# Kernel tuning notes

Measured on AMD Instinct MI355X. Metric: run time of the kernel, lower is better.

Reference implementation:

```python
import jax, jax.numpy as jnp
import numpy as np

N = 50000
E = 800000
DIN = 64
DOUT = 64
H = 4
C = DOUT // H
EPS = 1e-5


def setup_inputs() -> dict:
    key = jax.random.key(0)
    ks = jax.random.split(key, 40)
    inp = {}
    inp["x"] = jax.random.normal(ks[0], (N, DIN), jnp.float32)
    inp["edge_index"] = jax.random.randint(ks[1], (2, E), 0, N, dtype=jnp.int32)
    inp["edge_weight"] = jax.random.uniform(ks[2], (E,), jnp.float32)
    inp["edge_attr"] = jax.random.normal(ks[3], (E, 1), jnp.float32)
    k = 4
    for i in range(2):
        din = DIN if i == 0 else DOUT
        s = din ** -0.5
        inp[f"gcn_w{i}"] = jax.random.normal(ks[k], (din, DOUT), jnp.float32) * s; k += 1
        inp[f"gcn_b{i}"] = jnp.zeros((DOUT,), jnp.float32)
        inp[f"res_w{i}"] = jax.random.normal(ks[k], (din, DOUT), jnp.float32) * s; k += 1
        inp[f"res_b{i}"] = jnp.zeros((DOUT,), jnp.float32)
        inp[f"ln_g{i}"] = jnp.ones((DOUT,), jnp.float32)
        inp[f"ln_b{i}"] = jnp.zeros((DOUT,), jnp.float32)
        sg = DOUT ** -0.5
        inp[f"gat_w{i}"] = jax.random.normal(ks[k], (DOUT, H * C), jnp.float32) * sg; k += 1
        inp[f"gat_b{i}"] = jnp.zeros((H * C,), jnp.float32)
        inp[f"att_src{i}"] = jax.random.normal(ks[k], (H, C), jnp.float32) * (C ** -0.5); k += 1
        inp[f"att_dst{i}"] = jax.random.normal(ks[k], (H, C), jnp.float32) * (C ** -0.5); k += 1
        inp[f"att_e{i}"] = jax.random.normal(ks[k], (H, C), jnp.float32) * (C ** -0.5); k += 1
        inp[f"ew_w{i}"] = jax.random.normal(ks[k], (1, H * C), jnp.float32); k += 1
    return inp


def _gcn(x, src0, dst0, ew, W, b):
    n = x.shape[0]
    sl = jnp.arange(n, dtype=src0.dtype)
    src = jnp.concatenate([src0, sl])
    dst = jnp.concatenate([dst0, sl])
    w = jnp.concatenate([ew, jnp.ones((n,), ew.dtype)])  # self-loop weight 1
    deg = jax.ops.segment_sum(w, dst, num_segments=n)
    dinv = jnp.where(deg > 0, jax.lax.rsqrt(deg), 0.0)
    norm = dinv[src] * w * dinv[dst]
    h = x @ W  # [n, DOUT]
    out = jax.ops.segment_sum(h[src] * norm[:, None], dst, num_segments=n)
    return out + b


def _gat(x, src0, dst0, ea, W, b, a_src, a_dst, a_e, We):
    n = x.shape[0]
    sl = jnp.arange(n, dtype=src0.dtype)
    src = jnp.concatenate([src0, sl])
    dst = jnp.concatenate([dst0, sl])
    loop_attr = jnp.broadcast_to(ea.mean(axis=0, keepdims=True), (n, ea.shape[1]))
    ea2 = jnp.concatenate([ea, loop_attr], axis=0)  # fill_value='mean'
    xl = (x @ W).reshape(n, H, C)
    a_s = (xl * a_src).sum(-1)  # [n,H]
    a_d = (xl * a_dst).sum(-1)
    a_ee = ((ea2 @ We).reshape(-1, H, C) * a_e).sum(-1)  # [E2,H]
    alpha = jax.nn.leaky_relu(a_s[src] + a_d[dst] + a_ee, 0.2)
    m = jax.ops.segment_max(alpha, dst, num_segments=n)
    e = jnp.exp(alpha - m[dst])
    s = jax.ops.segment_sum(e, dst, num_segments=n)
    alpha = e / (s[dst] + 1e-16)
    out = jax.ops.segment_sum(xl[src] * alpha[:, :, None], dst, num_segments=n)
    return out.reshape(n, H * C) + b


def _ln(x, g, b):
    mu = x.mean(-1, keepdims=True)
    v = ((x - mu) ** 2).mean(-1, keepdims=True)
    return (x - mu) * jax.lax.rsqrt(v + EPS) * g + b


def reference(x, edge_index, edge_weight, edge_attr,
              gcn_w0, gcn_b0, res_w0, res_b0, ln_g0, ln_b0,
              gat_w0, gat_b0, att_src0, att_dst0, att_e0, ew_w0,
              gcn_w1, gcn_b1, res_w1, res_b1, ln_g1, ln_b1,
              gat_w1, gat_b1, att_src1, att_dst1, att_e1, ew_w1):
    src0, dst0 = edge_index[0], edge_index[1]
    layers = [
        (gcn_w0, gcn_b0, res_w0, res_b0, ln_g0, ln_b0, gat_w0, gat_b0, att_src0, att_dst0, att_e0, ew_w0),
        (gcn_w1, gcn_b1, res_w1, res_b1, ln_g1, ln_b1, gat_w1, gat_b1, att_src1, att_dst1, att_e1, ew_w1),
    ]
    for (gw, gb, rw, rb, lg, lb, Wg, bg, a_s, a_d, a_e, We) in layers:
        residual = x @ rw + rb
        x = jax.nn.silu(_gcn(x, src0, dst0, edge_weight, gw, gb)) + residual
        x = _ln(x, lg, lb)
        x = jax.nn.silu(_gat(x, src0, dst0, edge_attr, Wg, bg, a_s, a_d, a_e, We)) + x
    return x  # down_sample=False -> Identity
```

## Files before the change

kernel.cpp:

```cpp
#include <hip/hip_runtime.h>
#include <hip/hip_fp16.h>

#define NN 50000
#define NE 800000
#define D 64
#define EPS 1e-5f
#define NT 3125
#define NB1 250
#define EPB 3200
#define NBIN 196
#define STOT 49152
#define SBLK 192

typedef unsigned short ushort_t;
typedef unsigned int uint_t;
typedef __attribute__((ext_vector_type(8))) short bf16x8;
typedef __attribute__((ext_vector_type(4))) float f32x4;

__device__ __forceinline__ float wave_sum64(float v) {
#pragma unroll
  for (int m = 1; m <= 32; m <<= 1) v += __shfl_xor(v, m, 64);
  return v;
}
__device__ __forceinline__ float group_sum16(float v) {
#pragma unroll
  for (int m = 1; m <= 8; m <<= 1) v += __shfl_xor(v, m, 64);
  return v;
}
__device__ __forceinline__ float silu_f(float v) { return v / (1.f + __expf(-v)); }
__device__ __forceinline__ float lrelu_f(float v) { return v >= 0.f ? v : 0.2f * v; }
__device__ __forceinline__ ushort_t f2b(float x) {
  unsigned u = __float_as_uint(x);
  return (ushort_t)((u + 0x7FFFu + ((u >> 16) & 1u)) >> 16);
}
__device__ __forceinline__ float b2f(ushort_t u) {
  return __uint_as_float(((unsigned)u) << 16);
}
__device__ __forceinline__ ushort_t f2h(float x) {
  return __half_as_ushort(__float2half_rn(x));
}
__device__ __forceinline__ float h2f(unsigned u) {
  return __half2float(__ushort_as_half((ushort_t)(u & 0xFFFFu)));
}
__device__ __forceinline__ float sel4(float a, float b, float c, float d, int h) {
  float ab = (h & 1) ? b : a;
  float cd = (h & 1) ? d : c;
  return (h & 2) ? cd : ab;
}
__device__ __forceinline__ bf16x8 pack8(float4 a, float4 b) {
  bf16x8 r;
  r[0] = (short)f2b(a.x); r[1] = (short)f2b(a.y);
  r[2] = (short)f2b(a.z); r[3] = (short)f2b(a.w);
  r[4] = (short)f2b(b.x); r[5] = (short)f2b(b.y);
  r[6] = (short)f2b(b.z); r[7] = (short)f2b(b.w);
  return r;
}


__global__ void __launch_bounds__(256) k_hist196(const int* __restrict__ ei,
                                                 int* __restrict__ histG) {
  __shared__ int h[NBIN];
  int blk = blockIdx.x;
  for (int j = threadIdx.x; j < NBIN; j += 256) h[j] = 0;
  __syncthreads();
  int e0 = blk * EPB;
  for (int e = e0 + threadIdx.x; e < e0 + EPB; e += 256)
    atomicAdd(&h[ei[NE + e] >> 8], 1);
  __syncthreads();
  for (int j = threadIdx.x; j < NBIN; j += 256) histG[j * NB1 + blk] = h[j];
}

__global__ void __launch_bounds__(256) k_scanMA(int* __restrict__ histG,
                                                int* __restrict__ bsum) {
  __shared__ int sm[256];
  int j = threadIdx.x;
  int i = blockIdx.x * 256 + j;
  const int TOT = NBIN * NB1;
  int v = (i < TOT) ? histG[i] : 0;
  sm[j] = v;
  __syncthreads();
  for (int off = 1; off < 256; off <<= 1) {
    int t = (j >= off) ? sm[j - off] : 0;
    __syncthreads();
    sm[j] += t;
    __syncthreads();
  }
  if (i < TOT) histG[i] = sm[j] - v;
  if (j == 255) bsum[blockIdx.x] = sm[255];
}

__global__ void __launch_bounds__(256) k_scanMB(int* __restrict__ bsum,
                                                float* __restrict__ scal) {
  __shared__ int sm[256];
  int j = threadIdx.x;
  for (int t = j; t < 1024; t += 256) scal[t] = 0.f;
  int v = (j < SBLK) ? bsum[j] : 0;
  sm[j] = v;
  __syncthreads();
  for (int off = 1; off < 256; off <<= 1) {
    int t = (j >= off) ? sm[j - off] : 0;
    __syncthreads();
    sm[j] += t;
    __syncthreads();
  }
  if (j < SBLK) bsum[j] = sm[j] - v;
}

__global__ void __launch_bounds__(256) k_scanMC(int* __restrict__ histG,
                                                const int* __restrict__ bsum) {
  int i = blockIdx.x * 256 + threadIdx.x;
  const int TOT = NBIN * NB1;
  if (i < TOT) histG[i] += bsum[i >> 8];
}

__global__ void __launch_bounds__(256) k_part(
    const int* __restrict__ ei, const float* __restrict__ ew,
    const float* __restrict__ ea, const int* __restrict__ histG,
    uint2* __restrict__ rectmp, float* __restrict__ scal) {
  __shared__ int cur[NBIN];
  int blk = blockIdx.x;
  for (int j = threadIdx.x; j < NBIN; j += 256) cur[j] = histG[j * NB1 + blk];
  __syncthreads();
  int e0 = blk * EPB;
  float asum = 0.f;
  for (int e = e0 + threadIdx.x; e < e0 + EPB; e += 256) {
    int src = ei[e];
    int dst = ei[NE + e];
    float w = ew[e];
    float a = ea[e];
    asum += a;
    int slot = atomicAdd(&cur[dst >> 8], 1);
    uint2 r;
    r.x = (uint_t)(src & 0xFFFF) | ((uint_t)f2h(w) << 16);
    r.y = (uint_t)(dst & 0xFF) | ((uint_t)f2h(a) << 16);
    rectmp[slot] = r;
  }
  float s = wave_sum64(asum);
  if ((threadIdx.x & 63) == 0) {
    int slot = (blk * 4 + (threadIdx.x >> 6)) & 63;
    atomicAdd(&scal[(size_t)slot * 16], s);
  }
}

__global__ void __launch_bounds__(256) k_sortfin(
    const uint2* __restrict__ rectmp, const int* __restrict__ histG,
    uint2* __restrict__ rec, int* __restrict__ rs) {
  __shared__ int cnt[256], sc[256], cur[256];
  int b = blockIdx.x;
  int t = threadIdx.x;
  int lo = histG[b * NB1];
  int hi = (b == NBIN - 1) ? NE : histG[(b + 1) * NB1];
  cnt[t] = 0;
  __syncthreads();
  for (int e = lo + t; e < hi; e += 256)
    atomicAdd(&cnt[rectmp[e].y & 0xFFu], 1);
  __syncthreads();
  int v = cnt[t];
  sc[t] = v;
  __syncthreads();
  for (int off = 1; off < 256; off <<= 1) {
    int u = (t >= off) ? sc[t - off] : 0;
    __syncthreads();
    sc[t] += u;
    __syncthreads();
  }
  int ex = sc[t] - v;
  int node = b * 256 + t;
  if (node < NN) rs[node] = lo + ex;
  if (b == NBIN - 1 && t == 0) rs[NN] = NE;
  cur[t] = lo + ex;
  __syncthreads();
  for (int e = lo + t; e < hi; e += 256) {
    uint2 r = rectmp[e];
    int dl = (int)(r.y & 0xFFu);
    int slot = atomicAdd(&cur[dl], 1);
    uint_t src = r.x & 0xFFFFu;
    uint2 o;
    o.x = r.x;
    o.y = src | (r.y & 0xFFFF0000u);
    rec[slot] = o;
  }
}

__global__ void k_deg(const uint_t* __restrict__ rec, const int* __restrict__ rs,
                      float* __restrict__ dinv, float* __restrict__ scal) {
  int i = blockIdx.x * blockDim.x + threadIdx.x;
  if (i < NN) {
    float s = 1.f;
    int k1 = rs[i + 1];
    for (int k = rs[i]; k < k1; ++k) s += h2f(rec[2 * k] >> 16);
    dinv[i] = rsqrtf(s);
  }
  if (i == 0) {
    float t = 0.f;
    for (int j = 0; j < 64; ++j) t += scal[(size_t)j * 16];
    scal[1] = t / (float)NE;
  }
}

__global__ void __launch_bounds__(256) k_dual_gemm(
    const float* __restrict__ x, const float* __restrict__ W1,
    const float* __restrict__ W2, const float* __restrict__ b2,
    ushort_t* __restrict__ out1, float* __restrict__ out2) {
  __shared__ ushort_t wf[2 * 2 * 4 * 512];
  for (int e = threadIdx.x; e < 8192; e += 256) {
    int f = e >> 9, r = e & 511;
    int lane = r >> 3, j = r & 7;
    int m = f >> 3, s = (f >> 2) & 1, t = f & 3;
    int k = s * 32 + (lane >> 4) * 8 + j;
    int n = t * 16 + (lane & 15);
    const float* Wm = m ? W2 : W1;
    wf[e] = f2b(Wm[k * D + n]);
  }
  __syncthreads();
  int tile = blockIdx.x * 4 + (threadIdx.x >> 6);
  if (tile >= NT) return;
  int l = threadIdx.x & 63;
  int q = l >> 4, cn = l & 15;
  const float* xr = x + ((size_t)tile * 16 + cn) * D + q * 8;
  float4 xa = *(const float4*)xr;
  float4 xb = *(const float4*)(xr + 4);
  float4 xc = *(const float4*)(xr + 32);
  float4 xd = *(const float4*)(xr + 36);
  bf16x8 a0 = pack8(xa, xb), a1 = pack8(xc, xd);
  f32x4 acc1[4], acc2[4];
#pragma unroll
  for (int t = 0; t < 4; ++t) {
    bf16x8 b10 = *(const bf16x8*)&wf[(0 * 8 + 0 * 4 + t) * 512 + l * 8];
    bf16x8 b11 = *(const bf16x8*)&wf[(0 * 8 + 1 * 4 + t) * 512 + l * 8];
    bf16x8 b20 = *(const bf16x8*)&wf[(1 * 8 + 0 * 4 + t) * 512 + l * 8];
    bf16x8 b21 = *(const bf16x8*)&wf[(1 * 8 + 1 * 4 + t) * 512 + l * 8];
    f32x4 z = {0.f, 0.f, 0.f, 0.f};
    acc1[t] = __builtin_amdgcn_mfma_f32_16x16x32_bf16(a0, b10, z, 0, 0, 0);
    acc1[t] = __builtin_amdgcn_mfma_f32_16x16x32_bf16(a1, b11, acc1[t], 0, 0, 0);
    acc2[t] = __builtin_amdgcn_mfma_f32_16x16x32_bf16(a0, b20, z, 0, 0, 0);
    acc2[t] = __builtin_amdgcn_mfma_f32_16x16x32_bf16(a1, b21, acc2[t], 0, 0, 0);
  }
#pragma unroll
  for (int t = 0; t < 4; ++t) {
    float bb = b2[t * 16 + cn];
#pragma unroll
    for (int r = 0; r < 4; ++r) {
      size_t row = (size_t)tile * 16 + q * 4 + r;
      out1[row * D + t * 16 + cn] = f2b(acc1[t][r]);
      out2[row * D + t * 16 + cn] = acc2[t][r] + bb;
    }
  }
}

__global__ void __launch_bounds__(256) k_gat_node(
    const float* __restrict__ x2, const float* __restrict__ Wg,
    const float* __restrict__ att_src, const float* __restrict__ att_dst,
    const float* __restrict__ We, const float* __restrict__ a_e,
    ushort_t* __restrict__ xl, float* __restrict__ a_s, float* __restrict__ a_d,
    float* __restrict__ wea) {
  __shared__ ushort_t wf[2 * 4 * 512];
  for (int e = threadIdx.x; e < 4096; e += 256) {
    int f = e >> 9, r = e & 511;
    int lane = r >> 3, j = r & 7;
    int s = (f >> 2) & 1, t = f & 3;
    int k = s * 32 + (lane >> 4) * 8 + j;
    int n = t * 16 + (lane & 15);
    wf[e] = f2b(Wg[k * D + n]);
  }
  __syncthreads();
  if (blockIdx.x == 0 && threadIdx.x < 64) {
    int c = threadIdx.x;
    float v = group_sum16(We[c] * a_e[c]);
    if ((c & 15) == 0) wea[c >> 4] = v;
  }
  int tile = blockIdx.x * 4 + (threadIdx.x >> 6);
  if (tile >= NT) return;
  int l = threadIdx.x & 63;
  int q = l >> 4, cn = l & 15;
  const float* xr = x2 + ((size_t)tile * 16 + cn) * D + q * 8;
  float4 xa = *(const float4*)xr;
  float4 xb = *(const float4*)(xr + 4);
  float4 xc = *(const float4*)(xr + 32);
  float4 xd = *(const float4*)(xr + 36);
  bf16x8 a0 = pack8(xa, xb), a1 = pack8(xc, xd);
  f32x4 acc[4];
#pragma unroll
  for (int t = 0; t < 4; ++t) {
    bf16x8 b0 = *(const bf16x8*)&wf[(0 * 4 + t) * 512 + l * 8];
    bf16x8 b1 = *(const bf16x8*)&wf[(1 * 4 + t) * 512 + l * 8];
    f32x4 z = {0.f, 0.f, 0.f, 0.f};
    acc[t] = __builtin_amdgcn_mfma_f32_16x16x32_bf16(a0, b0, z, 0, 0, 0);
    acc[t] = __builtin_amdgcn_mfma_f32_16x16x32_bf16(a1, b1, acc[t], 0, 0, 0);
  }
#pragma unroll
  for (int t = 0; t < 4; ++t) {
    float av = att_src[t * 16 + cn];
    float dv = att_dst[t * 16 + cn];
#pragma unroll
    for (int r = 0; r < 4; ++r) {
      size_t row = (size_t)tile * 16 + q * 4 + r;
      xl[row * D + t * 16 + cn] = f2b(acc[t][r]);
      float vs = group_sum16(acc[t][r] * av);
      float vd = group_sum16(acc[t][r] * dv);
      if (cn == 0) {
        a_s[row * 4 + t] = vs;
        a_d[row * 4 + t] = vd;
      }
    }
  }
}


__global__ void __launch_bounds__(256) k_gcn_agg(
    const ushort_t* __restrict__ h16, const float* __restrict__ res,
    const float* __restrict__ dinv, const int* __restrict__ rs,
    const uint_t* __restrict__ rec,
    const float* __restrict__ gb, const float* __restrict__ lg, const float* __restrict__ lb,
    float* __restrict__ x2, int n) {
  __shared__ int   ss[4][64];
  __shared__ float swt[4][64];
  int w = threadIdx.x >> 6;
  int wv = (blockIdx.x * blockDim.x + threadIdx.x) >> 6;
  int iA = wv * 2;
  if (iA >= n) return;
  int iB = iA + 1;
  int l = threadIdx.x & 63;
  int half = l >> 5, cp = l & 31;
  float diA = dinv[iA], diB = dinv[iB];
  float accA = diA * diA * b2f(h16[(size_t)iA * D + l]);
  float accB = diB * diB * b2f(h16[(size_t)iB * D + l]);
  int kA = rs[iA], kA1 = rs[iA + 1];
  int kB = rs[iB], kB1 = rs[iB + 1];
  while (kA < kA1 || kB < kB1) {
    int cntA = min(32, kA1 - kA);
    int cntB = min(32, kB1 - kB);
    int src = 0; float wn = 0.f;
    if (half == 0) {
      if (cp < cntA) {
        uint_t r = rec[2 * (size_t)(kA + cp)];
        src = (int)(r & 0xFFFFu);
        wn = dinv[src] * h2f(r >> 16) * diA;
      }
    } else {
      if (cp < cntB) {
        uint_t r = rec[2 * (size_t)(kB + cp)];
        src = (int)(r & 0xFFFFu);
        wn = dinv[src] * h2f(r >> 16) * diB;
      }
    }
    ss[w][l] = src;
    swt[w][l] = wn;
    int nm = max(cntA, cntB);
    int j = 0;
    for (; j + 4 <= nm; j += 4) {
      int4 sa = *(const int4*)&ss[w][j];
      int4 sb = *(const int4*)&ss[w][32 + j];
      float4 wa = *(const float4*)&swt[w][j];
      float4 wb = *(const float4*)&swt[w][32 + j];
      float a0 = b2f(h16[(size_t)sa.x * D + l]);
      float b0 = b2f(h16[(size_t)sb.x * D + l]);
      float a1 = b2f(h16[(size_t)sa.y * D + l]);
      float b1 = b2f(h16[(size_t)sb.y * D + l]);
      float a2 = b2f(h16[(size_t)sa.z * D + l]);
      float b2v = b2f(h16[(size_t)sb.z * D + l]);
      float a3 = b2f(h16[(size_t)sa.w * D + l]);
      float b3 = b2f(h16[(size_t)sb.w * D + l]);
      accA = fmaf(wa.x, a0, accA); accB = fmaf(wb.x, b0, accB);
      accA = fmaf(wa.y, a1, accA); accB = fmaf(wb.y, b1, accB);
      accA = fmaf(wa.z, a2, accA); accB = fmaf(wb.z, b2v, accB);
      accA = fmaf(wa.w, a3, accA); accB = fmaf(wb.w, b3, accB);
    }
    for (; j < nm; ++j) {
      int sA = ss[w][j], sB = ss[w][32 + j];
      float wA = swt[w][j], wB = swt[w][32 + j];
      float vA = b2f(h16[(size_t)sA * D + l]);
      float vB = b2f(h16[(size_t)sB * D + l]);
      accA = fmaf(wA, vA, accA);
      accB = fmaf(wB, vB, accB);
    }
    kA += cntA; kB += cntB;
  }
  float gbv = gb[l], lgv = lg[l], lbv = lb[l];
  float x1A = silu_f(accA + gbv) + res[(size_t)iA * D + l];
  float x1B = silu_f(accB + gbv) + res[(size_t)iB * D + l];
  float muA = wave_sum64(x1A) * (1.f / 64.f);
  float muB = wave_sum64(x1B) * (1.f / 64.f);
  float dA = x1A - muA, dB = x1B - muB;
  float varA = wave_sum64(dA * dA) * (1.f / 64.f);
  float varB = wave_sum64(dB * dB) * (1.f / 64.f);
  x2[(size_t)iA * D + l] = dA * rsqrtf(varA + EPS) * lgv + lbv;
  x2[(size_t)iB * D + l] = dB * rsqrtf(varB + EPS) * lgv + lbv;
}

__global__ void __launch_bounds__(256) k_gat_agg(
    const ushort_t* __restrict__ xl16, const float* __restrict__ x2,
    const float* __restrict__ a_s, const float* __restrict__ a_d,
    const int* __restrict__ rs, const uint_t* __restrict__ rec,
    const float* __restrict__ wea, const float* __restrict__ scal,
    const float* __restrict__ bg, float* __restrict__ xout, int n) {
  __shared__ int   ss[4][64];
  __shared__ float el[4][4][68];
  int w = threadIdx.x >> 6;
  int wv = (blockIdx.x * blockDim.x + threadIdx.x) >> 6;
  int iA = wv * 2;
  if (iA >= n) return;
  int iB = iA + 1;
  int l = threadIdx.x & 63;
  int half = l >> 5, cp = l & 31;
  int hh = l >> 4;
  float4 wv4 = *(const float4*)wea;
  float mean_attr = scal[1];
  float we_h = sel4(wv4.x, wv4.y, wv4.z, wv4.w, hh);
  float ad_hA = a_d[(size_t)iA * 4 + hh], as_iA = a_s[(size_t)iA * 4 + hh];
  float ad_hB = a_d[(size_t)iB * 4 + hh], as_iB = a_s[(size_t)iB * 4 + hh];
  float eSA = __expf(lrelu_f(as_iA + ad_hA + mean_attr * we_h));
  float eSB = __expf(lrelu_f(as_iB + ad_hB + mean_attr * we_h));
  float sA = eSA, sB = eSB;
  float accA = eSA * b2f(xl16[(size_t)iA * D + l]);
  float accB = eSB * b2f(xl16[(size_t)iB * D + l]);
  const float* adp = a_d + (size_t)(half ? iB : iA) * 4;
  float4 ad4 = *(const float4*)adp;
  int kA = rs[iA], kA1 = rs[iA + 1];
  int kB = rs[iB], kB1 = rs[iB + 1];
  while (kA < kA1 || kB < kB1) {
    int cntA = min(32, kA1 - kA);
    int cntB = min(32, kB1 - kB);
    int myk = half ? kB : kA;
    int mycnt = half ? cntB : cntA;
    int src = 0;
    float e0v = 0.f, e1v = 0.f, e2v = 0.f, e3v = 0.f;
    if (cp < mycnt) {
      uint_t r = rec[2 * (size_t)(myk + cp) + 1];
      src = (int)(r & 0xFFFFu);
      float ea = h2f(r >> 16);
      float4 as4 = *(const float4*)(a_s + (size_t)src * 4);
      e0v = __expf(lrelu_f(as4.x + fmaf(ea, wv4.x, ad4.x)));
      e1v = __expf(lrelu_f(as4.y + fmaf(ea, wv4.y, ad4.y)));
      e2v = __expf(lrelu_f(as4.z + fmaf(ea, wv4.z, ad4.z)));
      e3v = __expf(lrelu_f(as4.w + fmaf(ea, wv4.w, ad4.w)));
    }
    ss[w][l] = src;
    el[w][0][l] = e0v;
    el[w][1][l] = e1v;
    el[w][2][l] = e2v;
    el[w][3][l] = e3v;
    int nm = max(cntA, cntB);
    int j = 0;
    for (; j + 4 <= nm; j += 4) {
      int4 sa = *(const int4*)&ss[w][j];
      int4 sb = *(const int4*)&ss[w][32 + j];
      float4 ea4 = *(const float4*)&el[w][hh][j];
      float4 eb4 = *(const float4*)&el[w][hh][32 + j];
      float a0 = b2f(xl16[(size_t)sa.x * D + l]);
      float b0 = b2f(xl16[(size_t)sb.x * D + l]);
      float a1 = b2f(xl16[(size_t)sa.y * D + l]);
      float b1 = b2f(xl16[(size_t)sb.y * D + l]);
      float a2 = b2f(xl16[(size_t)sa.z * D + l]);
      float b2v = b2f(xl16[(size_t)sb.z * D + l]);
      float a3 = b2f(xl16[(size_t)sa.w * D + l]);
      float b3 = b2f(xl16[(size_t)sb.w * D + l]);
      accA = fmaf(ea4.x, a0, accA); accB = fmaf(eb4.x, b0, accB);
      accA = fmaf(ea4.y, a1, accA); accB = fmaf(eb4.y, b1, accB);
      accA = fmaf(ea4.z, a2, accA); accB = fmaf(eb4.z, b2v, accB);
      accA = fmaf(ea4.w, a3, accA); accB = fmaf(eb4.w, b3, accB);
      sA += (ea4.x + ea4.y) + (ea4.z + ea4.w);
      sB += (eb4.x + eb4.y) + (eb4.z + eb4.w);
    }
    for (; j < nm; ++j) {
      int srcA = ss[w][j], srcB = ss[w][32 + j];
      float eA = el[w][hh][j], eB = el[w][hh][32 + j];
      float vA = b2f(xl16[(size_t)srcA * D + l]);
      float vB = b2f(xl16[(size_t)srcB * D + l]);
      accA = fmaf(eA, vA, accA);
      accB = fmaf(eB, vB, accB);
      sA += eA; sB += eB;
    }
    kA += cntA; kB += cntB;
  }
  float bgv = bg[l];
  float oA = accA / (sA + 1e-16f) + bgv;
  float oB = accB / (sB + 1e-16f) + bgv;
  xout[(size_t)iA * D + l] = silu_f(oA) + x2[(size_t)iA * D + l];
  xout[(size_t)iB * D + l] = silu_f(oB) + x2[(size_t)iB * D + l];
}


extern "C" void kernel_launch(void* const* d_in, const int* in_sizes, int n_in,
                              void* d_out, int out_size, void* d_ws, size_t ws_size,
                              hipStream_t stream) {
  (void)in_sizes; (void)n_in; (void)out_size; (void)ws_size;
  const float* x  = (const float*)d_in[0];
  const int*   ei = (const int*)d_in[1];
  const float* ew = (const float*)d_in[2];
  const float* ea = (const float*)d_in[3];
  const float* P[2][12];
  for (int l = 0; l < 2; ++l)
    for (int j = 0; j < 12; ++j) P[l][j] = (const float*)d_in[4 + l * 12 + j];

  float* W = (float*)d_ws;
  const size_t o_rs    = 0;
  const size_t o_dinv  = o_rs + NN + 16;
  const size_t o_wea   = o_dinv + NN;
  const size_t o_scal  = o_wea + 16;
  const size_t o_bsum  = o_scal + 1024;
  const size_t o_hist  = o_bsum + 256;
  const size_t o_rec   = o_hist + STOT;
  const size_t o_rtmp  = o_rec + (size_t)NE * 2;
  const size_t o_h16   = o_rtmp + (size_t)NE * 2;
  const size_t o_xl16  = o_h16 + (size_t)NN * D / 2;
  const size_t o_res   = o_xl16 + (size_t)NN * D / 2;
  const size_t o_x2    = o_res + (size_t)NN * D;
  const size_t o_xmid  = o_x2 + (size_t)NN * D;
  const size_t o_as    = o_xmid + (size_t)NN * D;
  const size_t o_ad    = o_as + (size_t)NN * 4;

  int*      rs    = (int*)(W + o_rs);
  float*    dinv  = W + o_dinv;
  float*    wea   = W + o_wea;
  float*    scal  = W + o_scal;
  int*      bsum  = (int*)(W + o_bsum);
  int*      histG = (int*)(W + o_hist);
  uint2*    rec   = (uint2*)(W + o_rec);
  uint2*    rtmp  = (uint2*)(W + o_rtmp);
  ushort_t* h16   = (ushort_t*)(W + o_h16);
  ushort_t* xl16  = (ushort_t*)(W + o_xl16);
  float*    resb  = W + o_res;
  float*    x2b   = W + o_x2;
  float*    xmid  = W + o_xmid;
  float*    asb   = W + o_as;
  float*    adb   = W + o_ad;

  const int B = 256;
  const int gN  = (NN + B - 1) / B;
  const int gN2 = ((NN / 2) * 64 + B - 1) / B;
  const int gMF = (NT + 3) / 4;

  k_hist196<<<NB1, B, 0, stream>>>(ei, histG);
  k_scanMA<<<SBLK, B, 0, stream>>>(histG, bsum);
  k_scanMB<<<1, B, 0, stream>>>(bsum, scal);
  k_scanMC<<<SBLK, B, 0, stream>>>(histG, bsum);
  k_part<<<NB1, B, 0, stream>>>(ei, ew, ea, histG, rtmp, scal);
  k_sortfin<<<NBIN, B, 0, stream>>>(rtmp, histG, rec, rs);
  k_deg<<<gN, B, 0, stream>>>((const uint_t*)rec, rs, dinv, scal);

  const float* xin = x;
  for (int l = 0; l < 2; ++l) {
    float* xout = (l == 0) ? xmid : (float*)d_out;
    k_dual_gemm<<<gMF, B, 0, stream>>>(xin, P[l][0], P[l][2], P[l][3], h16, resb);
    k_gcn_agg<<<gN2, B, 0, stream>>>(h16, resb, dinv, rs, (const uint_t*)rec,
                                     P[l][1], P[l][4], P[l][5], x2b, NN);
    k_gat_node<<<gMF, B, 0, stream>>>(x2b, P[l][6], P[l][8], P[l][9],
                                      P[l][11], P[l][10], xl16, asb, adb, wea);
    k_gat_agg<<<gN2, B, 0, stream>>>(xl16, x2b, asb, adb, rs, (const uint_t*)rec,
                                     wea, scal, P[l][7], xout, NN);
    xin = xout;
  }
}
```

Baseline: 310.4 us.

## Fold scan offsets into consumers, fuse degree into sort, precompute GCN edge norms

Removes the separate scan-add kernel by adding block offsets where the histogram is read in the partition and sort kernels. Computes node degrees inside the sort kernel with shared-memory atomics instead of a separate per-node degree pass. Adds a kernel that rewrites each edge's fp16 weight into the symmetric-normalized weight once, so both GCN layers skip the dinv gather per edge. Storing the normalized weight in fp16 changes rounding slightly, and the GAT aggregation must not rely on the original edge weight stored in the record.

Result: slower. 321.5 us (+3.6%).

```diff
diff --git a/kernel.cpp b/kernel.cpp
--- a/kernel.cpp
+++ b/kernel.cpp
@@ -9,7 +9,6 @@
 #define NB1 250
 #define EPB 3200
 #define NBIN 196
-#define STOT 49152
 #define SBLK 192
 
 typedef unsigned short ushort_t;
@@ -106,20 +105,17 @@
   if (j < SBLK) bsum[j] = sm[j] - v;
 }
 
-__global__ void __launch_bounds__(256) k_scanMC(int* __restrict__ histG,
-                                                const int* __restrict__ bsum) {
-  int i = blockIdx.x * 256 + threadIdx.x;
-  const int TOT = NBIN * NB1;
-  if (i < TOT) histG[i] += bsum[i >> 8];
-}
-
 __global__ void __launch_bounds__(256) k_part(
     const int* __restrict__ ei, const float* __restrict__ ew,
     const float* __restrict__ ea, const int* __restrict__ histG,
-    uint2* __restrict__ rectmp, float* __restrict__ scal) {
+    const int* __restrict__ bsum, uint2* __restrict__ rectmp,
+    float* __restrict__ scal) {
   __shared__ int cur[NBIN];
   int blk = blockIdx.x;
-  for (int j = threadIdx.x; j < NBIN; j += 256) cur[j] = histG[j * NB1 + blk];
+  for (int j = threadIdx.x; j < NBIN; j += 256) {
+    int idx = j * NB1 + blk;
+    cur[j] = histG[idx] + bsum[idx >> 8];
+  }
   __syncthreads();
   int e0 = blk * EPB;
   float asum = 0.f;
@@ -144,13 +140,21 @@
 
 __global__ void __launch_bounds__(256) k_sortfin(
     const uint2* __restrict__ rectmp, const int* __restrict__ histG,
-    uint2* __restrict__ rec, int* __restrict__ rs) {
+    const int* __restrict__ bsum, uint2* __restrict__ rec, int* __restrict__ rs,
+    float* __restrict__ dinv, float* __restrict__ scal) {
   __shared__ int cnt[256], sc[256], cur[256];
+  __shared__ float degs[256];
   int b = blockIdx.x;
   int t = threadIdx.x;
-  int lo = histG[b * NB1];
-  int hi = (b == NBIN - 1) ? NE : histG[(b + 1) * NB1];
+  int i0 = b * NB1;
+  int lo = histG[i0] + bsum[i0 >> 8];
+  int hi = NE;
+  if (b < NBIN - 1) {
+    int i1 = (b + 1) * NB1;
+    hi = histG[i1] + bsum[i1 >> 8];
+  }
   cnt[t] = 0;
+  degs[t] = 1.f;
   __syncthreads();
   for (int e = lo + t; e < hi; e += 256)
     atomicAdd(&cnt[rectmp[e].y & 0xFFu], 1);
@@ -179,22 +183,29 @@
     o.x = r.x;
     o.y = src | (r.y & 0xFFFF0000u);
     rec[slot] = o;
-  }
-}
-
-__global__ void k_deg(const uint_t* __restrict__ rec, const int* __restrict__ rs,
-                      float* __restrict__ dinv, float* __restrict__ scal) {
+    atomicAdd(&degs[dl], h2f(r.x >> 16));
+  }
+  __syncthreads();
+  if (node < NN) dinv[node] = rsqrtf(degs[t]);
+  if (b == 0 && t == 0) {
+    float s = 0.f;
+    for (int j = 0; j < 64; ++j) s += scal[(size_t)j * 16];
+    scal[1] = s / (float)NE;
+  }
+}
+
+__global__ void k_norm(uint2* __restrict__ rec, const int* __restrict__ rs,
+                       const float* __restrict__ dinv) {
   int i = blockIdx.x * blockDim.x + threadIdx.x;
-  if (i < NN) {
-    float s = 1.f;
-    int k1 = rs[i + 1];
-    for (int k = rs[i]; k < k1; ++k) s += h2f(rec[2 * k] >> 16);
-    dinv[i] = rsqrtf(s);
-  }
-  if (i == 0) {
-    float t = 0.f;
-    for (int j = 0; j < 64; ++j) t += scal[(size_t)j * 16];
-    scal[1] = t / (float)NE;
+  if (i >= NN) return;
+  float di = dinv[i];
+  int k1 = rs[i + 1];
+  for (int k = rs[i]; k < k1; ++k) {
+    uint2 r = rec[k];
+    int src = (int)(r.x & 0xFFFFu);
+    float wn = dinv[src] * h2f(r.x >> 16) * di;
+    r.x = (r.x & 0xFFFFu) | ((uint_t)f2h(wn) << 16);
+    rec[k] = r;
   }
 }
 
@@ -331,18 +342,12 @@
     int cntA = min(32, kA1 - kA);
     int cntB = min(32, kB1 - kB);
     int src = 0; float wn = 0.f;
-    if (half == 0) {
-      if (cp < cntA) {
-        uint_t r = rec[2 * (size_t)(kA + cp)];
-        src = (int)(r & 0xFFFFu);
-        wn = dinv[src] * h2f(r >> 16) * diA;
-      }
-    } else {
-      if (cp < cntB) {
-        uint_t r = rec[2 * (size_t)(kB + cp)];
-        src = (int)(r & 0xFFFFu);
-        wn = dinv[src] * h2f(r >> 16) * diB;
-      }
+    int myk = half ? kB : kA;
+    int mycnt = half ? cntB : cntA;
+    if (cp < mycnt) {
+      uint_t r = rec[2 * (size_t)(myk + cp)];
+      src = (int)(r & 0xFFFFu);
+      wn = h2f(r >> 16);
     }
     ss[w][l] = src;
     swt[w][l] = wn;
@@ -500,7 +505,7 @@
   const size_t o_scal  = o_wea + 16;
   const size_t o_bsum  = o_scal + 1024;
   const size_t o_hist  = o_bsum + 256;
-  const size_t o_rec   = o_hist + STOT;
+  const size_t o_rec   = o_hist + 49152;
   const size_t o_rtmp  = o_rec + (size_t)NE * 2;
   const size_t o_h16   = o_rtmp + (size_t)NE * 2;
   const size_t o_xl16  = o_h16 + (size_t)NN * D / 2;
@@ -534,10 +539,9 @@
   k_hist196<<<NB1, B, 0, stream>>>(ei, histG);
   k_scanMA<<<SBLK, B, 0, stream>>>(histG, bsum);
   k_scanMB<<<1, B, 0, stream>>>(bsum, scal);
-  k_scanMC<<<SBLK, B, 0, stream>>>(histG, bsum);
-  k_part<<<NB1, B, 0, stream>>>(ei, ew, ea, histG, rtmp, scal);
-  k_sortfin<<<NBIN, B, 0, stream>>>(rtmp, histG, rec, rs);
-  k_deg<<<gN, B, 0, stream>>>((const uint_t*)rec, rs, dinv, scal);
+  k_part<<<NB1, B, 0, stream>>>(ei, ew, ea, histG, bsum, rtmp, scal);
+  k_sortfin<<<NBIN, B, 0, stream>>>(rtmp, histG, bsum, rec, rs, dinv, scal);
+  k_norm<<<gN, B, 0, stream>>>(rec, rs, dinv);
 
   const float* xin = x;
   for (int l = 0; l < 2; ++l) {
```
